# Performance work log

Measured on AMD Instinct MI355X. Metric: run time of the kernel, lower is better.

## Reference

```python
import jax, jax.numpy as jnp
import numpy as np

LN_EPS = 1e-5  # torch.nn.LayerNorm default

def g(x):
    # minGRU activation: x + 0.5 for x >= 0, sigmoid(x) otherwise (always positive)
    return jnp.where(x >= 0, x + 0.5, jax.nn.sigmoid(x))

def log_g(x):
    return jnp.where(x >= 0, jnp.log(jax.nn.relu(x) + 0.5), -jax.nn.softplus(-x))

def layernorm(x, gamma, beta):
    mu = jnp.mean(x, axis=-1, keepdims=True)
    var = jnp.var(x, axis=-1, keepdims=True)
    return (x - mu) * jax.lax.rsqrt(var + LN_EPS) * gamma + beta

def mingru_scan(gate, hidden, h0):
    # gate, hidden: (B,S,D); h0: (B,1,D) positive
    # z = sigmoid(gate); h_t = (1-z_t)*h_{t-1} + z_t * g(hidden_t)
    # evaluated via Heinsen parallel scan in log space
    log_z = -jax.nn.softplus(-gate)          # log sigmoid(gate)
    log_coeffs = -jax.nn.softplus(gate)      # log(1 - sigmoid(gate))
    log_h0 = jnp.log(h0)                     # (B,1,D)
    log_tilde_h = log_g(hidden)
    a_star = jnp.cumsum(
        jnp.concatenate([jnp.zeros_like(log_h0), log_coeffs], axis=1), axis=1
    )                                        # (B,S+1,D)
    log_vals = jnp.concatenate([log_h0, log_z + log_tilde_h], axis=1) - a_star
    log_h = a_star + jax.lax.cumlogsumexp(log_vals, axis=1)
    return jnp.exp(log_h)[:, 1:]             # (B,S,D)

def setup_inputs() -> dict:
    key = jax.random.key(0)
    k1, k2 = jax.random.split(key)
    B, S, D, L = 8, 4096, 1024, 3
    x = jax.random.normal(k1, (B, S, D), dtype=jnp.float32)
    W = jax.random.normal(k2, (L, D, 2 * D), dtype=jnp.float32) * 0.02
    b = jnp.zeros((L, 2 * D), dtype=jnp.float32)
    ln_gamma = jnp.ones((L, D), dtype=jnp.float32)
    ln_beta = jnp.zeros((L, D), dtype=jnp.float32)
    return {"x": x, "ln_gamma": ln_gamma, "ln_beta": ln_beta, "W": W, "b": b}

def reference(x, ln_gamma, ln_beta, W, b):
    B, S, D = x.shape
    L = W.shape[0]
    inp = x
    next_hidden = []
    for l in range(L):
        h_prev = jnp.full((B, 1, D), 0.5, dtype=x.dtype)  # g(zeros) = 0.5
        xn = layernorm(inp, ln_gamma[l], ln_beta[l])
        gh = jnp.einsum('bsd,de->bse', xn, W[l]) + b[l]   # (B,S,2D)
        gate, hidden = jnp.split(gh, 2, axis=2)
        out = mingru_scan(gate, hidden, h_prev)
        next_hidden.append(out[:, -1:])
        out = out + inp  # residual (sizes equal -> identity res_align)
        inp = out
    return (out, *next_hidden)
```

## Files before the change

kernel.cpp:

```cpp
#include <hip/hip_runtime.h>

typedef unsigned short u16;
typedef unsigned int   u32;
typedef float  f32x2  __attribute__((ext_vector_type(2)));
typedef float  f32x4  __attribute__((ext_vector_type(4)));
typedef short  bf16x8 __attribute__((ext_vector_type(8)));
typedef u16    u16x4  __attribute__((ext_vector_type(4)));
typedef u32    u32x4  __attribute__((ext_vector_type(4)));

#define BQ 8
#define SQ 4096
#define DQ 1024
#define NQ 2048
#define MQ 32768
#define KQ 1024
#define CCH 128
#define TCH 32
#define NT 16

__device__ __forceinline__ float bf2f(u16 u){
  union { u32 i; float f; } v; v.i = ((u32)u) << 16; return v.f;
}
__device__ __forceinline__ u16 f2bf(float f){
  union { float f; u32 i; } v; v.f = f;
  u32 r = v.i + 0x7fffu + ((v.i >> 16) & 1u);
  return (u16)(r >> 16);
}

__device__ __forceinline__ void sig_ab(float gate, float hid, float& a, float& bv){
  float eg = __expf(gate);
  float a_ = __builtin_amdgcn_rcpf(1.f + eg);
  float z  = 1.f - a_;
  float eh = __expf(hid);
  float sg = eh * __builtin_amdgcn_rcpf(1.f + eh);
  float gval = (hid >= 0.f) ? (hid + 0.5f) : sg;
  a = a_; bv = z * gval;
}

__device__ __forceinline__ void gload_lds16(const u16* g, u16* l){
  __builtin_amdgcn_global_load_lds(
      (const __attribute__((address_space(1))) u32*)g,
      (__attribute__((address_space(3)))       u32*)l,
      16, 0, 0);
}

__global__ __launch_bounds__(256) void wt_cast(const float* __restrict__ W,
                                               u16* __restrict__ WT){
  __shared__ float t[64][65];
  const int l  = blockIdx.z;
  const int k0 = blockIdx.x << 6, n0 = blockIdx.y << 6;
  const float* Wl = W  + (size_t)l * KQ * NQ;
  u16*         Tl = WT + (size_t)l * NQ * KQ;
  const int c = threadIdx.x & 63, r4 = threadIdx.x >> 6;
  #pragma unroll
  for (int i = 0; i < 16; ++i){
    int r = i * 4 + r4;
    t[r][c] = Wl[(size_t)(k0 + r) * NQ + n0 + c];
  }
  __syncthreads();
  #pragma unroll
  for (int i = 0; i < 16; ++i){
    int r = i * 4 + r4;
    Tl[(size_t)(n0 + r) * KQ + k0 + c] = f2bf(t[c][r]);
  }
}

__global__ __launch_bounds__(256) void ln_cast(const float* __restrict__ x,
                                               const float* __restrict__ gamma,
                                               const float* __restrict__ beta,
                                               u16* __restrict__ xn){
  const size_t row = blockIdx.x;
  const int tid = threadIdx.x;
  f32x4 xv = *(const f32x4*)(x + row * DQ + tid * 4);
  float s  = xv[0] + xv[1] + xv[2] + xv[3];
  float s2 = xv[0]*xv[0] + xv[1]*xv[1] + xv[2]*xv[2] + xv[3]*xv[3];
  #pragma unroll
  for (int off = 32; off > 0; off >>= 1){
    s  += __shfl_down(s,  off);
    s2 += __shfl_down(s2, off);
  }
  __shared__ float red[8];
  const int wave = tid >> 6, lane = tid & 63;
  if (lane == 0){ red[wave] = s; red[4 + wave] = s2; }
  __syncthreads();
  s  = red[0] + red[1] + red[2] + red[3];
  s2 = red[4] + red[5] + red[6] + red[7];
  const float mean = s * (1.f / DQ);
  float var = fmaxf(s2 * (1.f / DQ) - mean * mean, 0.f);
  const float rstd = rsqrtf(var + 1e-5f);
  f32x4 gv = *(const f32x4*)(gamma + tid * 4);
  f32x4 bv = *(const f32x4*)(beta  + tid * 4);
  u16x4 o;
  #pragma unroll
  for (int e = 0; e < 4; ++e) o[e] = f2bf((xv[e] - mean) * rstd * gv[e] + bv[e]);
  *(u16x4*)(xn + row * DQ + tid * 4) = o;
}

__global__ __launch_bounds__(512, 2) void gemm_k8(const u16* __restrict__ A,
                                                  const u16* __restrict__ Bt,
                                                  const float* __restrict__ bias,
                                                  u32* __restrict__ abv,
                                                  float* __restrict__ pq){
  __shared__ u16 lds[2][2][2][8192];
  const int bid = blockIdx.x;
  const int swz = ((bid & 7) << 7) | (bid >> 3);
  const int bn = swz & 7, bm = swz >> 3;
  const int m0 = bm << 8;
  const int tid = threadIdx.x;
  const int w = tid >> 6, lane = tid & 63;
  const int wr = w >> 2, wc = w & 3;
  const int lr = lane & 15, hi = lane >> 4;
  const int sl8 = lane >> 3;
  const int sslot = (lane & 7) ^ sl8;

  f32x4 acc[2][2][4][2] = {};
  bf16x8 afrA[4][2], afrB[4][2];
  bf16x8 bf0[2][2], bf1[2][2];

#define FENCE asm volatile("" ::: "memory")
#define BAR do { FENCE; __builtin_amdgcn_s_barrier(); FENCE; } while(0)
#define SB  __builtin_amdgcn_sched_barrier(0)

#define STAGE(op, hf, kt, pb_) do {                                            \
    const u16* gsrc_ = (op) ? Bt : A;                                          \
    const int rb_ = (op) ? ((bn << 7) + (hf) * 1024) : (m0 + ((hf) << 7));     \
    _Pragma("unroll")                                                          \
    for (int g_ = 0; g_ < 2; ++g_){                                            \
      const int row_ = (w << 4) + (g_ << 3) + sl8;                             \
      gload_lds16(gsrc_ + (size_t)(rb_ + row_) * KQ + ((kt) << 6) + (sslot << 3),\
                  &lds[pb_][op][hf][((w << 4) + (g_ << 3)) << 6]);             \
    }                                                                          \
  } while(0)

#define LDSRD(dst, base_, row_, slot_) do {                                    \
    const int r_ = (row_);                                                     \
    dst = *(const bf16x8*)((const char*)(base_) +                              \
          ((r_ << 7) + ((((slot_)) ^ (r_ & 7)) << 4)));                        \
  } while(0)

#define RD_A(dst, hf, buf_) do {                                               \
    const u16* Ah_ = &lds[buf_][0][hf][0];                                     \
    _Pragma("unroll")                                                          \
    for (int i_ = 0; i_ < 4; ++i_)                                             \
      _Pragma("unroll")                                                        \
      for (int kk_ = 0; kk_ < 2; ++kk_)                                        \
        LDSRD(dst[i_][kk_], Ah_, (wr << 6) + (i_ << 4) + lr, (kk_ << 2) + hi); \
  } while(0)

#define RD_B(dst, hf, buf_) do {                                               \
    const u16* Bh_ = &lds[buf_][1][hf][0];                                     \
    _Pragma("unroll")                                                          \
    for (int j_ = 0; j_ < 2; ++j_)                                             \
      _Pragma("unroll")                                                        \
      for (int kk_ = 0; kk_ < 2; ++kk_)                                        \
        LDSRD(dst[j_][kk_], Bh_, (wc << 5) + (j_ << 4) + lr, (kk_ << 2) + hi); \
  } while(0)

#define MM(qm, qn, AR, B) do {                                                 \
    SB;                                                                        \
    __builtin_amdgcn_s_setprio(1);                                             \
    _Pragma("unroll")                                                          \
    for (int kk_ = 0; kk_ < 2; ++kk_)                                          \
      _Pragma("unroll")                                                        \
      for (int i_ = 0; i_ < 4; ++i_)                                           \
        _Pragma("unroll")                                                      \
        for (int j_ = 0; j_ < 2; ++j_)                                         \
          acc[qm][qn][i_][j_] = __builtin_amdgcn_mfma_f32_16x16x32_bf16(       \
              AR[i_][kk_], B[j_][kk_], acc[qm][qn][i_][j_], 0, 0, 0);          \
    __builtin_amdgcn_s_setprio(0);                                             \
  } while(0)

  STAGE(1, 0, 0, 0); STAGE(0, 0, 0, 0); STAGE(1, 1, 0, 0); STAGE(0, 1, 0, 0);
  asm volatile("s_waitcnt vmcnt(4)" ::: "memory");
  BAR;
  RD_A(afrA, 0, 0); RD_B(bf0, 0, 0);

  for (int t = 0; t < NT; ++t){
    const int pb = t & 1, qb = pb ^ 1;
    const bool s = (t + 1 < NT);
    asm volatile("s_waitcnt vmcnt(2)" ::: "memory");
    BAR;
    if (s) STAGE(1, 0, t + 1, qb);
    RD_B(bf1, 1, pb);
    MM(0, 0, afrA, bf0);
    if (s) { asm volatile("s_waitcnt vmcnt(2)" ::: "memory"); }
    else   { asm volatile("s_waitcnt vmcnt(0)" ::: "memory"); }
    BAR;
    if (s) STAGE(0, 0, t + 1, qb);
    RD_A(afrB, 1, pb);
    MM(0, 1, afrA, bf1);
    if (s) STAGE(1, 1, t + 1, qb);
    MM(1, 0, afrB, bf0);
    if (s){
      asm volatile("s_waitcnt vmcnt(2)" ::: "memory");
      BAR;
      STAGE(0, 1, t + 1, qb);
      RD_A(afrA, 0, qb); RD_B(bf0, 0, qb);
    }
    MM(1, 1, afrB, bf1);
  }
#undef MM
#undef RD_B
#undef RD_A
#undef LDSRD
#undef STAGE
#undef SB

  const int dbase = (bn << 7) + (wc << 5) + lr;
  #pragma unroll
  for (int qm = 0; qm < 2; ++qm){
    const int row00 = m0 + (qm << 7) + (wr << 6);
    #pragma unroll
    for (int half = 0; half < 2; ++half){
      float chP[2] = {1.f, 1.f}, chQ[2] = {0.f, 0.f};
      #pragma unroll
      for (int ii = 0; ii < 2; ++ii){
        const int i = (half << 1) + ii;
        float sgP[2] = {1.f, 1.f}, sgQ[2] = {0.f, 0.f};
        #pragma unroll
        for (int r = 0; r < 4; ++r){
          const int row = row00 + (i << 4) + (hi << 2) + r;
          #pragma unroll
          for (int j = 0; j < 2; ++j){
            const int d = dbase + (j << 4);
            float gate = acc[qm][0][i][j][r] + bias[d];
            float hid  = acc[qm][1][i][j][r] + bias[1024 + d];
            float a, bv; sig_ab(gate, hid, a, bv);
            u32 pk;
            asm volatile("v_cvt_pk_bf16_f32 %0, %1, %2"
                         : "=v"(pk) : "v"(a), "v"(bv));
            abv[(size_t)row * 1024 + d] = pk;
            union { u32 u; float f; } ua, ub;
            ua.u = pk << 16; ub.u = pk & 0xffff0000u;
            sgQ[j] = ua.f * sgQ[j] + ub.f;
            sgP[j] *= ua.f;
          }
        }
        #pragma unroll
        for (int j = 0; j < 2; ++j){
          float p = sgP[j], q = sgQ[j];
          float p1 = __shfl_up(p, 16), q1 = __shfl_up(q, 16);
          if (hi >= 1){ q = p * q1 + q; p = p * p1; }
          float p2 = __shfl_up(p, 32), q2 = __shfl_up(q, 32);
          if (hi >= 2){ q = p * q2 + q; p = p * p2; }
          chQ[j] = p * chQ[j] + q;
          chP[j] = p * chP[j];
        }
      }
      if (hi == 3){
        const int rowb = row00 + (half << 5);
        const int bq = rowb >> 12, cq = (rowb >> 5) & (CCH - 1);
        #pragma unroll
        for (int j = 0; j < 2; ++j){
          const int d = dbase + (j << 4);
          f32x2 v; v[0] = chP[j]; v[1] = chQ[j];
          *(f32x2*)(pq + ((((size_t)(bq * CCH + cq)) << 10) + d) * 2) = v;
        }
      }
    }
  }
#undef BAR
#undef FENCE
}

__global__ __launch_bounds__(256) void scan2(const float* __restrict__ pq,
                                             float* __restrict__ hst,
                                             float* __restrict__ hlast){
  const int idx = blockIdx.x * 256 + threadIdx.x;
  const int b = idx >> 10, d = idx & 1023;
  float h = 0.5f;
  for (int c = 0; c < CCH; ++c){
    const size_t o = ((size_t)(b * CCH + c) << 10) + d;
    hst[o] = h;
    f32x2 v = *(const f32x2*)(pq + o * 2);
    h = v[0] * h + v[1];
  }
  hlast[idx] = h;
}

template<int MODE>
__global__ __launch_bounds__(256) void scan3f(const u32* __restrict__ abv,
                                              const float* __restrict__ hst,
                                              const void* __restrict__ inp,
                                              void* __restrict__ outp,
                                              u16* __restrict__ xn,
                                              const float* __restrict__ gamma,
                                              const float* __restrict__ beta){
  const int b = blockIdx.x >> 7;
  const int c = blockIdx.x & (CCH - 1);
  const int tid = threadIdx.x;
  const int d4 = tid << 2;
  const int wave = tid >> 6, lane = tid & 63;
  const size_t srow = (size_t)b * SQ + (size_t)c * TCH;
  const u32* base = abv + srow * 1024 + d4;
  const size_t o = ((size_t)blockIdx.x << 10) + d4;
  f32x4 h0v = *(const f32x4*)(hst + o);
  float h[4] = {h0v[0], h0v[1], h0v[2], h0v[3]};
  __shared__ float red[2][8];
  f32x4 gv = {}, bvv = {};
  if (MODE != 2){
    gv  = *(const f32x4*)(gamma + d4);
    bvv = *(const f32x4*)(beta  + d4);
  }
  for (int t = 0; t < TCH; ++t){
    u32x4 ab = *(const u32x4*)(base + (size_t)t * 1024);
    f32x4 iv;
    if (MODE == 0){
      iv = *(const f32x4*)((const float*)inp + (srow + t) * DQ + d4);
    } else {
      u16x4 ib = *(const u16x4*)((const u16*)inp + (srow + t) * DQ + d4);
      #pragma unroll
      for (int e = 0; e < 4; ++e) iv[e] = bf2f(ib[e]);
    }
    f32x4 ov;
    #pragma unroll
    for (int e = 0; e < 4; ++e){
      const float a  = bf2f((u16)(ab[e] & 0xffffu));
      const float bv = bf2f((u16)(ab[e] >> 16));
      h[e] = a * h[e] + bv;
      ov[e] = h[e] + iv[e];
    }
    if (MODE == 2){
      *(f32x4*)((float*)outp + (srow + t) * DQ + d4) = ov;
    } else {
      u16x4 ob;
      #pragma unroll
      for (int e = 0; e < 4; ++e) ob[e] = f2bf(ov[e]);
      *(u16x4*)((u16*)outp + (srow + t) * DQ + d4) = ob;
      float s  = ov[0] + ov[1] + ov[2] + ov[3];
      float s2 = ov[0]*ov[0] + ov[1]*ov[1] + ov[2]*ov[2] + ov[3]*ov[3];
      #pragma unroll
      for (int off = 32; off > 0; off >>= 1){
        s  += __shfl_down(s,  off);
        s2 += __shfl_down(s2, off);
      }
      const int rb = t & 1;
      if (lane == 0){ red[rb][wave] = s; red[rb][4 + wave] = s2; }
      __syncthreads();
      s  = red[rb][0] + red[rb][1] + red[rb][2] + red[rb][3];
      s2 = red[rb][4] + red[rb][5] + red[rb][6] + red[rb][7];
      const float mean = s * (1.f / DQ);
      float var = fmaxf(s2 * (1.f / DQ) - mean * mean, 0.f);
      const float rstd = rsqrtf(var + 1e-5f);
      u16x4 xo;
      #pragma unroll
      for (int e = 0; e < 4; ++e)
        xo[e] = f2bf((ov[e] - mean) * rstd * gv[e] + bvv[e]);
      *(u16x4*)(xn + (srow + t) * DQ + d4) = xo;
    }
  }
}

extern "C" void kernel_launch(void* const* d_in, const int* in_sizes, int n_in,
                              void* d_out, int out_size, void* d_ws, size_t ws_size,
                              hipStream_t stream) {
  const float* x     = (const float*)d_in[0];
  const float* gamma = (const float*)d_in[1];
  const float* beta  = (const float*)d_in[2];
  const float* W     = (const float*)d_in[3];
  const float* bias  = (const float*)d_in[4];
  float* out = (float*)d_out;

  char* ws = (char*)d_ws;
  const size_t ACT = (size_t)MQ * DQ * 4;
  u16*   bufA = (u16*)(ws);
  u16*   bufB = (u16*)(ws + ACT);
  u32*   abv  = (u32*)(ws + 2 * ACT);
  u16*   xn   = (u16*)(ws + 3 * ACT);
  u16*   WT   = (u16*)(ws + 3 * ACT + (size_t)MQ * DQ * 2);
  float* pq   = (float*)(ws + 3 * ACT + (size_t)MQ * DQ * 2 + (size_t)3 * NQ * KQ * 2);
  float* hst  = pq + (size_t)2 * BQ * CCH * DQ;

  wt_cast<<<dim3(KQ / 64, NQ / 64, 3), 256, 0, stream>>>(W, WT);

  const dim3 ggrid((NQ / 256) * (MQ / 256));
  ln_cast<<<MQ, 256, 0, stream>>>(x, gamma, beta, xn);
  gemm_k8<<<ggrid, 512, 0, stream>>>(xn, WT, bias, abv, pq);
  scan2<<<(BQ * DQ) / 256, 256, 0, stream>>>(pq, hst, out + (size_t)MQ * DQ);
  scan3f<0><<<BQ * CCH, 256, 0, stream>>>(abv, hst, x, bufA, xn,
                                          gamma + DQ, beta + DQ);
  gemm_k8<<<ggrid, 512, 0, stream>>>(xn, WT + (size_t)NQ * KQ, bias + NQ,
                                     abv, pq);
  scan2<<<(BQ * DQ) / 256, 256, 0, stream>>>(pq, hst,
                                             out + (size_t)MQ * DQ + BQ * DQ);
  scan3f<1><<<BQ * CCH, 256, 0, stream>>>(abv, hst, bufA, bufB, xn,
                                          gamma + 2 * DQ, beta + 2 * DQ);
  gemm_k8<<<ggrid, 512, 0, stream>>>(xn, WT + (size_t)2 * NQ * KQ, bias + 2 * NQ,
                                     abv, pq);
  scan2<<<(BQ * DQ) / 256, 256, 0, stream>>>(pq, hst,
                                             out + (size_t)MQ * DQ + 2 * BQ * DQ);
  scan3f<2><<<BQ * CCH, 256, 0, stream>>>(abv, hst, bufB, out, nullptr,
                                          nullptr, nullptr);
}
```

Before: 716.1 us.

## Restructure chunked scan: smaller chunks, one wave per chunk, prefetched loads

Halves the scan chunk length (TCH 32->16, CCH 128->256), so the GEMM epilogue emits per-16-row chunk summaries and drops the cross-half combine. The final scan kernel maps one wave to one chunk covering all 1024 features, doing the LayerNorm reduction with wave-level xor shuffles instead of a block-wide syncthreads per timestep. It also software-prefetches the next timestep's loads. scan2 batches 16 chunk loads before its serial recurrence to expose memory parallelism. The GEMM's sched_barrier before each MFMA group is removed. Costs are more chunk summaries, more registers per thread in scan3f, and a longer serial chain in scan2.

```diff
diff --git a/kernel.cpp b/kernel.cpp
--- a/kernel.cpp
+++ b/kernel.cpp
@@ -14,8 +14,8 @@
 #define NQ 2048
 #define MQ 32768
 #define KQ 1024
-#define CCH 128
-#define TCH 32
+#define CCH 256
+#define TCH 16
 #define NT 16
 
 __device__ __forceinline__ float bf2f(u16 u){
@@ -119,7 +119,6 @@
 
 #define FENCE asm volatile("" ::: "memory")
 #define BAR do { FENCE; __builtin_amdgcn_s_barrier(); FENCE; } while(0)
-#define SB  __builtin_amdgcn_sched_barrier(0)
 
 #define STAGE(op, hf, kt, pb_) do {                                            \
     const u16* gsrc_ = (op) ? Bt : A;                                          \
@@ -157,7 +156,6 @@
   } while(0)
 
 #define MM(qm, qn, AR, B) do {                                                 \
-    SB;                                                                        \
     __builtin_amdgcn_s_setprio(1);                                             \
     _Pragma("unroll")                                                          \
     for (int kk_ = 0; kk_ < 2; ++kk_)                                          \
@@ -204,56 +202,49 @@
 #undef RD_A
 #undef LDSRD
 #undef STAGE
-#undef SB
 
   const int dbase = (bn << 7) + (wc << 5) + lr;
   #pragma unroll
   for (int qm = 0; qm < 2; ++qm){
     const int row00 = m0 + (qm << 7) + (wr << 6);
     #pragma unroll
-    for (int half = 0; half < 2; ++half){
-      float chP[2] = {1.f, 1.f}, chQ[2] = {0.f, 0.f};
-      #pragma unroll
-      for (int ii = 0; ii < 2; ++ii){
-        const int i = (half << 1) + ii;
-        float sgP[2] = {1.f, 1.f}, sgQ[2] = {0.f, 0.f};
-        #pragma unroll
-        for (int r = 0; r < 4; ++r){
-          const int row = row00 + (i << 4) + (hi << 2) + r;
-          #pragma unroll
-          for (int j = 0; j < 2; ++j){
-            const int d = dbase + (j << 4);
-            float gate = acc[qm][0][i][j][r] + bias[d];
-            float hid  = acc[qm][1][i][j][r] + bias[1024 + d];
-            float a, bv; sig_ab(gate, hid, a, bv);
-            u32 pk;
-            asm volatile("v_cvt_pk_bf16_f32 %0, %1, %2"
-                         : "=v"(pk) : "v"(a), "v"(bv));
-            abv[(size_t)row * 1024 + d] = pk;
-            union { u32 u; float f; } ua, ub;
-            ua.u = pk << 16; ub.u = pk & 0xffff0000u;
-            sgQ[j] = ua.f * sgQ[j] + ub.f;
-            sgP[j] *= ua.f;
-          }
-        }
-        #pragma unroll
-        for (int j = 0; j < 2; ++j){
-          float p = sgP[j], q = sgQ[j];
-          float p1 = __shfl_up(p, 16), q1 = __shfl_up(q, 16);
-          if (hi >= 1){ q = p * q1 + q; p = p * p1; }
-          float p2 = __shfl_up(p, 32), q2 = __shfl_up(q, 32);
-          if (hi >= 2){ q = p * q2 + q; p = p * p2; }
-          chQ[j] = p * chQ[j] + q;
-          chP[j] = p * chP[j];
-        }
-      }
-      if (hi == 3){
-        const int rowb = row00 + (half << 5);
-        const int bq = rowb >> 12, cq = (rowb >> 5) & (CCH - 1);
+    for (int i = 0; i < 4; ++i){
+      float sgP[2] = {1.f, 1.f}, sgQ[2] = {0.f, 0.f};
+      #pragma unroll
+      for (int r = 0; r < 4; ++r){
+        const int row = row00 + (i << 4) + (hi << 2) + r;
         #pragma unroll
         for (int j = 0; j < 2; ++j){
           const int d = dbase + (j << 4);
-          f32x2 v; v[0] = chP[j]; v[1] = chQ[j];
+          float gate = acc[qm][0][i][j][r] + bias[d];
+          float hid  = acc[qm][1][i][j][r] + bias[1024 + d];
+          float a, bv; sig_ab(gate, hid, a, bv);
+          u32 pk;
+          asm volatile("v_cvt_pk_bf16_f32 %0, %1, %2"
+                       : "=v"(pk) : "v"(a), "v"(bv));
+          abv[(size_t)row * 1024 + d] = pk;
+          union { u32 u; float f; } ua, ub;
+          ua.u = pk << 16; ub.u = pk & 0xffff0000u;
+          sgQ[j] = ua.f * sgQ[j] + ub.f;
+          sgP[j] *= ua.f;
+        }
+      }
+      #pragma unroll
+      for (int j = 0; j < 2; ++j){
+        float p = sgP[j], q = sgQ[j];
+        float p1 = __shfl_up(p, 16), q1 = __shfl_up(q, 16);
+        if (hi >= 1){ q = p * q1 + q; p = p * p1; }
+        float p2 = __shfl_up(p, 32), q2 = __shfl_up(q, 32);
+        if (hi >= 2){ q = p * q2 + q; p = p * p2; }
+        sgP[j] = p; sgQ[j] = q;
+      }
+      if (hi == 3){
+        const int rowb = row00 + (i << 4);
+        const int bq = rowb >> 12, cq = (rowb >> 4) & (CCH - 1);
+        #pragma unroll
+        for (int j = 0; j < 2; ++j){
+          const int d = dbase + (j << 4);
+          f32x2 v; v[0] = sgP[j]; v[1] = sgQ[j];
           *(f32x2*)(pq + ((((size_t)(bq * CCH + cq)) << 10) + d) * 2) = v;
         }
       }
@@ -269,11 +260,17 @@
   const int idx = blockIdx.x * 256 + threadIdx.x;
   const int b = idx >> 10, d = idx & 1023;
   float h = 0.5f;
-  for (int c = 0; c < CCH; ++c){
-    const size_t o = ((size_t)(b * CCH + c) << 10) + d;
-    hst[o] = h;
-    f32x2 v = *(const f32x2*)(pq + o * 2);
-    h = v[0] * h + v[1];
+  const size_t cb = ((size_t)b * CCH) << 10;
+  for (int cg = 0; cg < CCH / 16; ++cg){
+    f32x2 v[16];
+    #pragma unroll
+    for (int k = 0; k < 16; ++k)
+      v[k] = *(const f32x2*)(pq + (cb + ((size_t)(cg * 16 + k) << 10) + d) * 2);
+    #pragma unroll
+    for (int k = 0; k < 16; ++k){
+      hst[cb + ((size_t)(cg * 16 + k) << 10) + d] = h;
+      h = v[k][0] * h + v[k][1];
+    }
   }
   hlast[idx] = h;
 }
@@ -286,69 +283,95 @@
                                               u16* __restrict__ xn,
                                               const float* __restrict__ gamma,
                                               const float* __restrict__ beta){
-  const int b = blockIdx.x >> 7;
-  const int c = blockIdx.x & (CCH - 1);
-  const int tid = threadIdx.x;
-  const int d4 = tid << 2;
-  const int wave = tid >> 6, lane = tid & 63;
+  const int wch = (blockIdx.x << 2) | (threadIdx.x >> 6);
+  const int b = wch >> 8;
+  const int c = wch & (CCH - 1);
+  const int lane = threadIdx.x & 63;
+  const int d0 = lane << 2;
   const size_t srow = (size_t)b * SQ + (size_t)c * TCH;
-  const u32* base = abv + srow * 1024 + d4;
-  const size_t o = ((size_t)blockIdx.x << 10) + d4;
-  f32x4 h0v = *(const f32x4*)(hst + o);
-  float h[4] = {h0v[0], h0v[1], h0v[2], h0v[3]};
-  __shared__ float red[2][8];
-  f32x4 gv = {}, bvv = {};
+  const u32* abase = abv + srow * 1024 + d0;
+
+  float h[4][4];
+  #pragma unroll
+  for (int q = 0; q < 4; ++q)
+    *(f32x4*)h[q] = *(const f32x4*)(hst + ((size_t)wch << 10) + d0 + q * 256);
+
+  f32x4 gv[4], bt[4];
   if (MODE != 2){
-    gv  = *(const f32x4*)(gamma + d4);
-    bvv = *(const f32x4*)(beta  + d4);
-  }
+    #pragma unroll
+    for (int q = 0; q < 4; ++q){
+      gv[q] = *(const f32x4*)(gamma + d0 + q * 256);
+      bt[q] = *(const f32x4*)(beta  + d0 + q * 256);
+    }
+  }
+
+  u32x4 abq[4], abn[4];
+  f32x4 ivq[4], ivn[4];
+#define LOADT(dstab, dstiv, t_) do {                                           \
+    _Pragma("unroll")                                                          \
+    for (int q_ = 0; q_ < 4; ++q_){                                            \
+      dstab[q_] = *(const u32x4*)(abase + (size_t)(t_) * 1024 + q_ * 256);     \
+      if (MODE == 0){                                                          \
+        dstiv[q_] = *(const f32x4*)((const float*)inp +                        \
+                     (srow + (t_)) * DQ + d0 + q_ * 256);                      \
+      } else {                                                                 \
+        u16x4 ib_ = *(const u16x4*)((const u16*)inp +                          \
+                     (srow + (t_)) * DQ + d0 + q_ * 256);                      \
+        _Pragma("unroll")                                                      \
+        for (int e_ = 0; e_ < 4; ++e_) dstiv[q_][e_] = bf2f(ib_[e_]);          \
+      }                                                                        \
+    }                                                                          \
+  } while(0)
+
+  LOADT(abq, ivq, 0);
   for (int t = 0; t < TCH; ++t){
-    u32x4 ab = *(const u32x4*)(base + (size_t)t * 1024);
-    f32x4 iv;
-    if (MODE == 0){
-      iv = *(const f32x4*)((const float*)inp + (srow + t) * DQ + d4);
+    if (t + 1 < TCH) LOADT(abn, ivn, t + 1);
+    f32x4 ov[4];
+    float s = 0.f, s2 = 0.f;
+    #pragma unroll
+    for (int q = 0; q < 4; ++q){
+      #pragma unroll
+      for (int e = 0; e < 4; ++e){
+        const float a  = bf2f((u16)(abq[q][e] & 0xffffu));
+        const float bv = bf2f((u16)(abq[q][e] >> 16));
+        h[q][e] = a * h[q][e] + bv;
+        ov[q][e] = h[q][e] + ivq[q][e];
+        s += ov[q][e]; s2 += ov[q][e] * ov[q][e];
+      }
+    }
+    if (MODE == 2){
+      #pragma unroll
+      for (int q = 0; q < 4; ++q)
+        *(f32x4*)((float*)outp + (srow + t) * DQ + d0 + q * 256) = ov[q];
     } else {
-      u16x4 ib = *(const u16x4*)((const u16*)inp + (srow + t) * DQ + d4);
-      #pragma unroll
-      for (int e = 0; e < 4; ++e) iv[e] = bf2f(ib[e]);
-    }
-    f32x4 ov;
-    #pragma unroll
-    for (int e = 0; e < 4; ++e){
-      const float a  = bf2f((u16)(ab[e] & 0xffffu));
-      const float bv = bf2f((u16)(ab[e] >> 16));
-      h[e] = a * h[e] + bv;
-      ov[e] = h[e] + iv[e];
-    }
-    if (MODE == 2){
-      *(f32x4*)((float*)outp + (srow + t) * DQ + d4) = ov;
-    } else {
-      u16x4 ob;
-      #pragma unroll
-      for (int e = 0; e < 4; ++e) ob[e] = f2bf(ov[e]);
-      *(u16x4*)((u16*)outp + (srow + t) * DQ + d4) = ob;
-      float s  = ov[0] + ov[1] + ov[2] + ov[3];
-      float s2 = ov[0]*ov[0] + ov[1]*ov[1] + ov[2]*ov[2] + ov[3]*ov[3];
+      #pragma unroll
+      for (int q = 0; q < 4; ++q){
+        u16x4 ob;
+        #pragma unroll
+        for (int e = 0; e < 4; ++e) ob[e] = f2bf(ov[q][e]);
+        *(u16x4*)((u16*)outp + (srow + t) * DQ + d0 + q * 256) = ob;
+      }
       #pragma unroll
       for (int off = 32; off > 0; off >>= 1){
-        s  += __shfl_down(s,  off);
-        s2 += __shfl_down(s2, off);
-      }
-      const int rb = t & 1;
-      if (lane == 0){ red[rb][wave] = s; red[rb][4 + wave] = s2; }
-      __syncthreads();
-      s  = red[rb][0] + red[rb][1] + red[rb][2] + red[rb][3];
-      s2 = red[rb][4] + red[rb][5] + red[rb][6] + red[rb][7];
+        s  += __shfl_xor(s,  off);
+        s2 += __shfl_xor(s2, off);
+      }
       const float mean = s * (1.f / DQ);
       float var = fmaxf(s2 * (1.f / DQ) - mean * mean, 0.f);
       const float rstd = rsqrtf(var + 1e-5f);
-      u16x4 xo;
-      #pragma unroll
-      for (int e = 0; e < 4; ++e)
-        xo[e] = f2bf((ov[e] - mean) * rstd * gv[e] + bvv[e]);
-      *(u16x4*)(xn + (srow + t) * DQ + d4) = xo;
-    }
-  }
+      #pragma unroll
+      for (int q = 0; q < 4; ++q){
+        u16x4 xo;
+        #pragma unroll
+        for (int e = 0; e < 4; ++e)
+          xo[e] = f2bf((ov[q][e] - mean) * rstd * gv[q][e] + bt[q][e]);
+        *(u16x4*)(xn + (srow + t) * DQ + d0 + q * 256) = xo;
+      }
+    }
+    #pragma unroll
+    for (int q = 0; q < 4; ++q){ abq[q] = abn[q]; ivq[q] = ivn[q]; }
+  }
+#undef LOADT
 }
 
 extern "C" void kernel_launch(void* const* d_in, const int* in_sizes, int n_in,
@@ -374,21 +397,22 @@
   wt_cast<<<dim3(KQ / 64, NQ / 64, 3), 256, 0, stream>>>(W, WT);
 
   const dim3 ggrid((NQ / 256) * (MQ / 256));
+  const int s3grid = (BQ * CCH) / 4;
   ln_cast<<<MQ, 256, 0, stream>>>(x, gamma, beta, xn);
   gemm_k8<<<ggrid, 512, 0, stream>>>(xn, WT, bias, abv, pq);
   scan2<<<(BQ * DQ) / 256, 256, 0, stream>>>(pq, hst, out + (size_t)MQ * DQ);
-  scan3f<0><<<BQ * CCH, 256, 0, stream>>>(abv, hst, x, bufA, xn,
-                                          gamma + DQ, beta + DQ);
+  scan3f<0><<<s3grid, 256, 0, stream>>>(abv, hst, x, bufA, xn,
+                                        gamma + DQ, beta + DQ);
   gemm_k8<<<ggrid, 512, 0, stream>>>(xn, WT + (size_t)NQ * KQ, bias + NQ,
                                      abv, pq);
   scan2<<<(BQ * DQ) / 256, 256, 0, stream>>>(pq, hst,
                                              out + (size_t)MQ * DQ + BQ * DQ);
-  scan3f<1><<<BQ * CCH, 256, 0, stream>>>(abv, hst, bufA, bufB, xn,
-                                          gamma + 2 * DQ, beta + 2 * DQ);
+  scan3f<1><<<s3grid, 256, 0, stream>>>(abv, hst, bufA, bufB, xn,
+                                        gamma + 2 * DQ, beta + 2 * DQ);
   gemm_k8<<<ggrid, 512, 0, stream>>>(xn, WT + (size_t)2 * NQ * KQ, bias + 2 * NQ,
                                      abv, pq);
   scan2<<<(BQ * DQ) / 256, 256, 0, stream>>>(pq, hst,
                                              out + (size_t)MQ * DQ + 2 * BQ * DQ);
-  scan3f<2><<<BQ * CCH, 256, 0, stream>>>(abv, hst, bufB, out, nullptr,
-                                          nullptr, nullptr);
-}
+  scan3f<2><<<s3grid, 256, 0, stream>>>(abv, hst, bufB, out, nullptr,
+                                        nullptr, nullptr);
+}
```

After: 745.2 us. 4.1% more time.

## Restructure GEMM main loop into deeper prefetch pipeline with per-quadrant barriers

Applied to the files above, without the earlier changes.

Reworks the LDS double-buffer schedule so global-to-LDS loads for tile t+2 are issued into the just-consumed buffer while tile t computes, with seven stages prefetched in the prologue. Each quadrant MFMA block is now bracketed by barriers and an explicit lgkmcnt(0) wait, and the sched_barrier hints are removed. The goal is to hide more global memory latency behind MFMA work. The cost is many more workgroup barriers per iteration and a more fragile ordering of buffer reuse.

```diff
diff --git a/kernel.cpp b/kernel.cpp
--- a/kernel.cpp
+++ b/kernel.cpp
@@ -119,7 +119,7 @@
 
 #define FENCE asm volatile("" ::: "memory")
 #define BAR do { FENCE; __builtin_amdgcn_s_barrier(); FENCE; } while(0)
-#define SB  __builtin_amdgcn_sched_barrier(0)
+#define LGKM0 asm volatile("s_waitcnt lgkmcnt(0)" ::: "memory")
 
 #define STAGE(op, hf, kt, pb_) do {                                            \
     const u16* gsrc_ = (op) ? Bt : A;                                          \
@@ -157,7 +157,6 @@
   } while(0)
 
 #define MM(qm, qn, AR, B) do {                                                 \
-    SB;                                                                        \
     __builtin_amdgcn_s_setprio(1);                                             \
     _Pragma("unroll")                                                          \
     for (int kk_ = 0; kk_ < 2; ++kk_)                                          \
@@ -170,41 +169,42 @@
     __builtin_amdgcn_s_setprio(0);                                             \
   } while(0)
 
-  STAGE(1, 0, 0, 0); STAGE(0, 0, 0, 0); STAGE(1, 1, 0, 0); STAGE(0, 1, 0, 0);
-  asm volatile("s_waitcnt vmcnt(4)" ::: "memory");
+  STAGE(0, 0, 0, 0); STAGE(1, 0, 0, 0); STAGE(0, 1, 0, 0); STAGE(1, 1, 0, 0);
+  STAGE(0, 0, 1, 1); STAGE(1, 0, 1, 1); STAGE(0, 1, 1, 1);
+  asm volatile("s_waitcnt vmcnt(6)" ::: "memory");
   BAR;
-  RD_A(afrA, 0, 0); RD_B(bf0, 0, 0);
 
   for (int t = 0; t < NT; ++t){
     const int pb = t & 1, qb = pb ^ 1;
-    const bool s = (t + 1 < NT);
-    asm volatile("s_waitcnt vmcnt(2)" ::: "memory");
-    BAR;
-    if (s) STAGE(1, 0, t + 1, qb);
+    const bool s1 = (t + 1 < NT), s2 = (t + 2 < NT);
+    RD_A(afrA, 0, pb); RD_B(bf0, 0, pb);
+    if (s1) STAGE(1, 1, t + 1, qb);
+    BAR; LGKM0;
+    MM(0, 0, afrA, bf0);
+    BAR;
     RD_B(bf1, 1, pb);
-    MM(0, 0, afrA, bf0);
-    if (s) { asm volatile("s_waitcnt vmcnt(2)" ::: "memory"); }
-    else   { asm volatile("s_waitcnt vmcnt(0)" ::: "memory"); }
-    BAR;
-    if (s) STAGE(0, 0, t + 1, qb);
+    if (s2) STAGE(0, 0, t + 2, pb);
+    BAR; LGKM0;
+    MM(0, 1, afrA, bf1);
+    BAR;
     RD_A(afrB, 1, pb);
-    MM(0, 1, afrA, bf1);
-    if (s) STAGE(1, 1, t + 1, qb);
+    if (s2) STAGE(1, 0, t + 2, pb);
+    BAR; LGKM0;
     MM(1, 0, afrB, bf0);
-    if (s){
-      asm volatile("s_waitcnt vmcnt(2)" ::: "memory");
-      BAR;
-      STAGE(0, 1, t + 1, qb);
-      RD_A(afrA, 0, qb); RD_B(bf0, 0, qb);
-    }
+    BAR;
+    if (s2) STAGE(0, 1, t + 2, pb);
+    BAR;
     MM(1, 1, afrB, bf1);
+    if (s2)      { asm volatile("s_waitcnt vmcnt(6)" ::: "memory"); }
+    else if (s1) { asm volatile("s_waitcnt vmcnt(0)" ::: "memory"); }
+    BAR;
   }
 #undef MM
 #undef RD_B
 #undef RD_A
 #undef LDSRD
 #undef STAGE
-#undef SB
+#undef LGKM0
 
   const int dbase = (bn << 7) + (wc << 5) + lr;
   #pragma unroll
```

Result: no change. 720.4 us (+0.6%).

## Fold LayerNorm into GEMM epilogue via gamma-scaled weights and column sums

Applied to the files above, without the earlier changes.

LayerNorm is applied algebraically after the GEMM. Gamma is folded into the bf16 weights, and precomputed column sums plus beta·W terms are used with per-row mean and rstd in the epilogue. This removes the separate normalized-activation write and read, and the block-wide barrier reduction in the scan kernels, which now only emit per-wave partial sums. The cost is extra setup kernels for column sums, more epilogue work per row, and numerical risk from subtracting mean*colsum on un-normalized bf16 inputs. It also removes the sched_barrier from the MFMA macro.

```diff
diff --git a/kernel.cpp b/kernel.cpp
--- a/kernel.cpp
+++ b/kernel.cpp
@@ -45,6 +45,7 @@
 }
 
 __global__ __launch_bounds__(256) void wt_cast(const float* __restrict__ W,
+                                               const float* __restrict__ gamma,
                                                u16* __restrict__ WT){
   __shared__ float t[64][65];
   const int l  = blockIdx.z;
@@ -58,20 +59,57 @@
     t[r][c] = Wl[(size_t)(k0 + r) * NQ + n0 + c];
   }
   __syncthreads();
+  const float g = gamma[l * DQ + k0 + c];
   #pragma unroll
   for (int i = 0; i < 16; ++i){
     int r = i * 4 + r4;
-    Tl[(size_t)(n0 + r) * KQ + k0 + c] = f2bf(t[c][r]);
-  }
-}
-
-__global__ __launch_bounds__(256) void ln_cast(const float* __restrict__ x,
+    Tl[(size_t)(n0 + r) * KQ + k0 + c] = f2bf(g * t[c][r]);
+  }
+}
+
+__global__ __launch_bounds__(256) void colpart(const float* __restrict__ W,
                                                const float* __restrict__ gamma,
                                                const float* __restrict__ beta,
-                                               u16* __restrict__ xn){
+                                               float* __restrict__ cp){
+  const int n = blockIdx.x * 256 + threadIdx.x;
+  const int seg = blockIdx.y, l = blockIdx.z;
+  const float* Wl = W + (size_t)l * KQ * NQ;
+  float cs = 0.f, cb = 0.f;
+  #pragma unroll 4
+  for (int k = seg * 128; k < seg * 128 + 128; ++k){
+    float w = Wl[(size_t)k * NQ + n];
+    cs += bf2f(f2bf(gamma[l * DQ + k] * w));
+    cb += beta[l * DQ + k] * w;
+  }
+  const size_t o = (((size_t)l * 8 + seg) * NQ + n) * 2;
+  cp[o] = cs; cp[o + 1] = cb;
+}
+__global__ __launch_bounds__(256) void colfin(const float* __restrict__ cp,
+                                              const float* __restrict__ bias,
+                                              float* __restrict__ colsum,
+                                              float* __restrict__ cbeta){
+  const int n = blockIdx.x * 256 + threadIdx.x;
+  const int l = blockIdx.y;
+  float cs = 0.f, cb = 0.f;
+  #pragma unroll
+  for (int seg = 0; seg < 8; ++seg){
+    const size_t o = (((size_t)l * 8 + seg) * NQ + n) * 2;
+    cs += cp[o]; cb += cp[o + 1];
+  }
+  colsum[l * NQ + n] = cs;
+  cbeta [l * NQ + n] = cb + bias[l * NQ + n];
+}
+
+__global__ __launch_bounds__(256) void x_cast(const float* __restrict__ x,
+                                              u16* __restrict__ bx,
+                                              float* __restrict__ stats){
   const size_t row = blockIdx.x;
-  const int tid = threadIdx.x;
+  const int tid = threadIdx.x, wave = tid >> 6, lane = tid & 63;
   f32x4 xv = *(const f32x4*)(x + row * DQ + tid * 4);
+  u16x4 o;
+  #pragma unroll
+  for (int e = 0; e < 4; ++e) o[e] = f2bf(xv[e]);
+  *(u16x4*)(bx + row * DQ + tid * 4) = o;
   float s  = xv[0] + xv[1] + xv[2] + xv[3];
   float s2 = xv[0]*xv[0] + xv[1]*xv[1] + xv[2]*xv[2] + xv[3]*xv[3];
   #pragma unroll
@@ -79,26 +117,17 @@
     s  += __shfl_down(s,  off);
     s2 += __shfl_down(s2, off);
   }
-  __shared__ float red[8];
-  const int wave = tid >> 6, lane = tid & 63;
-  if (lane == 0){ red[wave] = s; red[4 + wave] = s2; }
-  __syncthreads();
-  s  = red[0] + red[1] + red[2] + red[3];
-  s2 = red[4] + red[5] + red[6] + red[7];
-  const float mean = s * (1.f / DQ);
-  float var = fmaxf(s2 * (1.f / DQ) - mean * mean, 0.f);
-  const float rstd = rsqrtf(var + 1e-5f);
-  f32x4 gv = *(const f32x4*)(gamma + tid * 4);
-  f32x4 bv = *(const f32x4*)(beta  + tid * 4);
-  u16x4 o;
-  #pragma unroll
-  for (int e = 0; e < 4; ++e) o[e] = f2bf((xv[e] - mean) * rstd * gv[e] + bv[e]);
-  *(u16x4*)(xn + row * DQ + tid * 4) = o;
+  if (lane == 0){
+    f32x2 v; v[0] = s; v[1] = s2;
+    *(f32x2*)(stats + row * 8 + wave * 2) = v;
+  }
 }
 
 __global__ __launch_bounds__(512, 2) void gemm_k8(const u16* __restrict__ A,
                                                   const u16* __restrict__ Bt,
-                                                  const float* __restrict__ bias,
+                                                  const float* __restrict__ colsum,
+                                                  const float* __restrict__ cbeta,
+                                                  const float* __restrict__ stats,
                                                   u32* __restrict__ abv,
                                                   float* __restrict__ pq){
   __shared__ u16 lds[2][2][2][8192];
@@ -119,7 +148,6 @@
 
 #define FENCE asm volatile("" ::: "memory")
 #define BAR do { FENCE; __builtin_amdgcn_s_barrier(); FENCE; } while(0)
-#define SB  __builtin_amdgcn_sched_barrier(0)
 
 #define STAGE(op, hf, kt, pb_) do {                                            \
     const u16* gsrc_ = (op) ? Bt : A;                                          \
@@ -157,7 +185,6 @@
   } while(0)
 
 #define MM(qm, qn, AR, B) do {                                                 \
-    SB;                                                                        \
     __builtin_amdgcn_s_setprio(1);                                             \
     _Pragma("unroll")                                                          \
     for (int kk_ = 0; kk_ < 2; ++kk_)                                          \
@@ -204,9 +231,15 @@
 #undef RD_A
 #undef LDSRD
 #undef STAGE
-#undef SB
 
   const int dbase = (bn << 7) + (wc << 5) + lr;
+  float csg[2], csh[2], cbg[2], cbh[2];
+  #pragma unroll
+  for (int j = 0; j < 2; ++j){
+    const int d = dbase + (j << 4);
+    csg[j] = colsum[d];        csh[j] = colsum[1024 + d];
+    cbg[j] = cbeta[d];         cbh[j] = cbeta[1024 + d];
+  }
   #pragma unroll
   for (int qm = 0; qm < 2; ++qm){
     const int row00 = m0 + (qm << 7) + (wr << 6);
@@ -220,11 +253,18 @@
         #pragma unroll
         for (int r = 0; r < 4; ++r){
           const int row = row00 + (i << 4) + (hi << 2) + r;
+          f32x4 p0 = *(const f32x4*)(stats + (size_t)row * 8);
+          f32x4 p1 = *(const f32x4*)(stats + (size_t)row * 8 + 4);
+          const float ssum = p0[0] + p0[2] + p1[0] + p1[2];
+          const float ssq  = p0[1] + p0[3] + p1[1] + p1[3];
+          const float mean = ssum * (1.f / DQ);
+          const float var  = fmaxf(ssq * (1.f / DQ) - mean * mean, 0.f);
+          const float rstd = rsqrtf(var + 1e-5f);
           #pragma unroll
           for (int j = 0; j < 2; ++j){
             const int d = dbase + (j << 4);
-            float gate = acc[qm][0][i][j][r] + bias[d];
-            float hid  = acc[qm][1][i][j][r] + bias[1024 + d];
+            float gate = rstd * (acc[qm][0][i][j][r] - mean * csg[j]) + cbg[j];
+            float hid  = rstd * (acc[qm][1][i][j][r] - mean * csh[j]) + cbh[j];
             float a, bv; sig_ab(gate, hid, a, bv);
             u32 pk;
             asm volatile("v_cvt_pk_bf16_f32 %0, %1, %2"
@@ -283,9 +323,7 @@
                                               const float* __restrict__ hst,
                                               const void* __restrict__ inp,
                                               void* __restrict__ outp,
-                                              u16* __restrict__ xn,
-                                              const float* __restrict__ gamma,
-                                              const float* __restrict__ beta){
+                                              float* __restrict__ stats){
   const int b = blockIdx.x >> 7;
   const int c = blockIdx.x & (CCH - 1);
   const int tid = threadIdx.x;
@@ -296,12 +334,6 @@
   const size_t o = ((size_t)blockIdx.x << 10) + d4;
   f32x4 h0v = *(const f32x4*)(hst + o);
   float h[4] = {h0v[0], h0v[1], h0v[2], h0v[3]};
-  __shared__ float red[2][8];
-  f32x4 gv = {}, bvv = {};
-  if (MODE != 2){
-    gv  = *(const f32x4*)(gamma + d4);
-    bvv = *(const f32x4*)(beta  + d4);
-  }
   for (int t = 0; t < TCH; ++t){
     u32x4 ab = *(const u32x4*)(base + (size_t)t * 1024);
     f32x4 iv;
@@ -334,19 +366,10 @@
         s  += __shfl_down(s,  off);
         s2 += __shfl_down(s2, off);
       }
-      const int rb = t & 1;
-      if (lane == 0){ red[rb][wave] = s; red[rb][4 + wave] = s2; }
-      __syncthreads();
-      s  = red[rb][0] + red[rb][1] + red[rb][2] + red[rb][3];
-      s2 = red[rb][4] + red[rb][5] + red[rb][6] + red[rb][7];
-      const float mean = s * (1.f / DQ);
-      float var = fmaxf(s2 * (1.f / DQ) - mean * mean, 0.f);
-      const float rstd = rsqrtf(var + 1e-5f);
-      u16x4 xo;
-      #pragma unroll
-      for (int e = 0; e < 4; ++e)
-        xo[e] = f2bf((ov[e] - mean) * rstd * gv[e] + bvv[e]);
-      *(u16x4*)(xn + (srow + t) * DQ + d4) = xo;
+      if (lane == 0){
+        f32x2 v; v[0] = s; v[1] = s2;
+        *(f32x2*)(stats + (srow + t) * 8 + wave * 2) = v;
+      }
     }
   }
 }
@@ -362,33 +385,36 @@
   float* out = (float*)d_out;
 
   char* ws = (char*)d_ws;
-  const size_t ACT = (size_t)MQ * DQ * 4;
-  u16*   bufA = (u16*)(ws);
-  u16*   bufB = (u16*)(ws + ACT);
-  u32*   abv  = (u32*)(ws + 2 * ACT);
-  u16*   xn   = (u16*)(ws + 3 * ACT);
-  u16*   WT   = (u16*)(ws + 3 * ACT + (size_t)MQ * DQ * 2);
-  float* pq   = (float*)(ws + 3 * ACT + (size_t)MQ * DQ * 2 + (size_t)3 * NQ * KQ * 2);
-  float* hst  = pq + (size_t)2 * BQ * CCH * DQ;
-
-  wt_cast<<<dim3(KQ / 64, NQ / 64, 3), 256, 0, stream>>>(W, WT);
+  const size_t HALF = (size_t)MQ * DQ * 2;
+  u16*   bufX = (u16*)(ws);
+  u16*   bufA = (u16*)(ws + HALF);
+  u16*   bufB = (u16*)(ws + 2 * HALF);
+  u32*   abv  = (u32*)(ws + 3 * HALF);
+  u16*   WT   = (u16*)(ws + 5 * HALF);
+  float* pq   = (float*)(ws + 5 * HALF + (size_t)3 * NQ * KQ * 2);
+  float* hst  = pq  + (size_t)2 * BQ * CCH * DQ;
+  float* stats= hst + (size_t)BQ * CCH * DQ;
+  float* cpart= stats + (size_t)MQ * 8;
+  float* colsum = cpart + (size_t)3 * 8 * NQ * 2;
+  float* cbeta  = colsum + (size_t)3 * NQ;
+
+  wt_cast<<<dim3(KQ / 64, NQ / 64, 3), 256, 0, stream>>>(W, gamma, WT);
+  colpart<<<dim3(NQ / 256, 8, 3), 256, 0, stream>>>(W, gamma, beta, cpart);
+  colfin<<<dim3(NQ / 256, 3), 256, 0, stream>>>(cpart, bias, colsum, cbeta);
+  x_cast<<<MQ, 256, 0, stream>>>(x, bufX, stats);
 
   const dim3 ggrid((NQ / 256) * (MQ / 256));
-  ln_cast<<<MQ, 256, 0, stream>>>(x, gamma, beta, xn);
-  gemm_k8<<<ggrid, 512, 0, stream>>>(xn, WT, bias, abv, pq);
+  gemm_k8<<<ggrid, 512, 0, stream>>>(bufX, WT, colsum, cbeta, stats, abv, pq);
   scan2<<<(BQ * DQ) / 256, 256, 0, stream>>>(pq, hst, out + (size_t)MQ * DQ);
-  scan3f<0><<<BQ * CCH, 256, 0, stream>>>(abv, hst, x, bufA, xn,
-                                          gamma + DQ, beta + DQ);
-  gemm_k8<<<ggrid, 512, 0, stream>>>(xn, WT + (size_t)NQ * KQ, bias + NQ,
-                                     abv, pq);
+  scan3f<0><<<BQ * CCH, 256, 0, stream>>>(abv, hst, x, bufA, stats);
+  gemm_k8<<<ggrid, 512, 0, stream>>>(bufA, WT + (size_t)NQ * KQ,
+                                     colsum + NQ, cbeta + NQ, stats, abv, pq);
   scan2<<<(BQ * DQ) / 256, 256, 0, stream>>>(pq, hst,
                                              out + (size_t)MQ * DQ + BQ * DQ);
-  scan3f<1><<<BQ * CCH, 256, 0, stream>>>(abv, hst, bufA, bufB, xn,
-                                          gamma + 2 * DQ, beta + 2 * DQ);
-  gemm_k8<<<ggrid, 512, 0, stream>>>(xn, WT + (size_t)2 * NQ * KQ, bias + 2 * NQ,
-                                     abv, pq);
+  scan3f<1><<<BQ * CCH, 256, 0, stream>>>(abv, hst, bufA, bufB, stats);
+  gemm_k8<<<ggrid, 512, 0, stream>>>(bufB, WT + (size_t)2 * NQ * KQ,
+                                     colsum + 2 * NQ, cbeta + 2 * NQ, stats, abv, pq);
   scan2<<<(BQ * DQ) / 256, 256, 0, stream>>>(pq, hst,
                                              out + (size_t)MQ * DQ + 2 * BQ * DQ);
-  scan3f<2><<<BQ * CCH, 256, 0, stream>>>(abv, hst, bufB, out, nullptr,
-                                          nullptr, nullptr);
-}
+  scan3f<2><<<BQ * CCH, 256, 0, stream>>>(abv, hst, bufB, out, nullptr);
+}
```

Result: slower. 745.4 us (+4.1%).
